# Kernel optimization log

Hardware: AMD Instinct MI355X
Metric: run time of the kernel (lower is better)

The kernel has to match this reference:

```python
import jax, jax.numpy as jnp
import numpy as np

DECAY = 0.99   # LIF membrane decay
INH = 1.625    # lateral inhibition strength (mode='max')


def setup_inputs() -> dict:
    key = jax.random.key(0)
    kx, kw = jax.random.split(key)
    B, Cin, Cout = 8192, 4096, 1024
    x = (jax.random.uniform(kx, (B, Cin)) < 0.2).astype(jnp.float32)
    # weights, then normweight(): clamp to [0,1] and scale each row so row-max == 0.1
    W = jax.random.uniform(kw, (Cout, Cin), dtype=jnp.float32)
    W = W / (W.max(axis=1, keepdims=True) / 0.1)
    return {"x": x, "W": W, "time_window": 10}


def reference(x, W, time_window):
    # current through the bias-free linear layer; constant across timesteps
    i = x @ W.T                                   # (B, Cout)
    # adaptive threshold init: threshold = 3 * max over batch (thre_init branch)
    thr = 3.0 * i.max(axis=0)                     # (Cout,)
    imax = i.max(axis=1, keepdims=True)           # (B, 1), for mode='max' inhibition
    C = i.shape[1]

    def step(mem, _):
        mem = mem * DECAY + i                     # LIF integration
        s = (mem > thr).astype(i.dtype)           # threshold fire
        mem = mem * (1.0 - s)                     # hard reset at all spikers
        row = s.max(axis=1, keepdims=True)        # (B,1) 1 if any neuron in row spiked
        # winner-take-all k=1: keep a single spiking neuron per row (first/argmax)
        wta = jax.nn.one_hot(jnp.argmax(s, axis=1), C, dtype=i.dtype) * row
        # lateral inhibition: subtract inh * max-current from losers in rows that spiked
        mem = mem - INH * imax * (row - wta)
        return mem, wta

    mem0 = jnp.zeros_like(i)
    _, wtas = jax.lax.scan(step, mem0, None, length=time_window)
    return wtas.sum(axis=0)                       # accumulated spikes (B, Cout)
```

## Files before the change

### kernel.cpp

```cpp
#include <hip/hip_runtime.h>
#include <cstdint>

#define B_DIM 8192
#define CIN   4096
#define COUT  1024
#define NPLN  3072

constexpr double W_SCALE   = 83230720.0;
constexpr int    QMAX      = 8323072;
constexpr double INV_SCALE = 0.1 / 8323072.0;

using i32x4 = __attribute__((ext_vector_type(4))) int;

__device__ __forceinline__ void async_copy16(void* lds, const void* g) {
    auto l = (__attribute__((address_space(3))) void*)(uintptr_t)(lds);
    auto p = (const __attribute__((address_space(1))) void*)(uintptr_t)(g);
    __builtin_amdgcn_global_load_lds(p, l, 16, 0, 0);
}

__global__ void prep_x(const float* __restrict__ x, int8_t* __restrict__ Ai) {
    const size_t base = (size_t)blockIdx.x * 1024;
    const float4* xp = (const float4*)x;
    int* op = (int*)Ai;
#pragma unroll
    for (int s = 0; s < 4; ++s) {
        const size_t g = base + s * 256 + threadIdx.x;
        float4 v = xp[g];
        int r = (v.x != 0.f ? 1 : 0) | ((v.y != 0.f ? 1 : 0) << 8) |
                ((v.z != 0.f ? 1 : 0) << 16) | ((v.w != 0.f ? 1 : 0) << 24);
        op[g] = r;
    }
}

__global__ void prep_w(const float* __restrict__ W, int8_t* __restrict__ Bd,
                       unsigned long long* __restrict__ cm) {
    const int idx = blockIdx.x * 256 + threadIdx.x;
    float4 w = ((const float4*)W)[idx];
    float ws[4] = {w.x, w.y, w.z, w.w};
    char dg[3][4];
#pragma unroll
    for (int k = 0; k < 4; ++k) {
        int qv = __double2int_rn((double)ws[k] * W_SCALE);
        qv = max(0, min(QMAX, qv));
        int d0 = ((qv + 128) & 255) - 128; int tq = (qv - d0) >> 8;
        int d1 = ((tq + 128) & 255) - 128; int d2 = (tq - d1) >> 8;
        dg[0][k] = (char)d0; dg[1][k] = (char)d1; dg[2][k] = (char)d2;
    }
    const size_t off = (size_t)idx * 4;
#pragma unroll
    for (int p = 0; p < 3; ++p) {
        char4 c4; c4.x = dg[p][0]; c4.y = dg[p][1]; c4.z = dg[p][2]; c4.w = dg[p][3];
        *(char4*)(Bd + (size_t)p * COUT * CIN + off) = c4;
    }
    if (idx < COUT) cm[idx] = 0ull;
}

__global__ __launch_bounds__(256, 2) void gemm_i8(const int8_t* __restrict__ A,
                                                  const int8_t* __restrict__ Bm,
                                                  int* __restrict__ S) {
    __shared__ alignas(16) int8_t As[128 * 64];
    __shared__ alignas(16) int8_t Bs[128 * 64];
    const int tid  = threadIdx.x;
    const int lane = tid & 63;
    const int wave = tid >> 6;
    const int wr = wave >> 1, wc = wave & 1;
    const int bn = blockIdx.x, bm = blockIdx.y;

    const int r0  = tid >> 2;
    const int c0  = tid & 3;
    const int gc0 = c0 ^ ((r0 >> 1) & 3);
    const int r1  = r0 + 64;
    const int gc1 = c0 ^ ((r1 >> 1) & 3);
    const int8_t* Ag0 = A  + (size_t)(bm * 128 + r0) * CIN + gc0 * 16;
    const int8_t* Ag1 = A  + (size_t)(bm * 128 + r1) * CIN + gc1 * 16;
    const int8_t* Bg0 = Bm + (size_t)(bn * 128 + r0) * CIN + gc0 * 16;
    const int8_t* Bg1 = Bm + (size_t)(bn * 128 + r1) * CIN + gc1 * 16;
    int8_t* AsW = As + wave * 1024;
    int8_t* BsW = Bs + wave * 1024;

    const int mrow = lane & 15;
    const int q    = lane >> 4;
    const int sw   = (mrow >> 1) & 3;
    const int aoff = (wr * 64 + mrow) * 64 + (q ^ sw) * 16;
    const int boff = (wc * 64 + mrow) * 64 + (q ^ sw) * 16;

    i32x4 acc[4][4] = {};
    for (int kc = 0; kc < CIN; kc += 64) {
        __syncthreads();
        async_copy16(AsW,        Ag0 + kc);
        async_copy16(AsW + 4096, Ag1 + kc);
        async_copy16(BsW,        Bg0 + kc);
        async_copy16(BsW + 4096, Bg1 + kc);
        __syncthreads();
        i32x4 a[4], b[4];
#pragma unroll
        for (int t = 0; t < 4; ++t) a[t] = *(const i32x4*)(As + aoff + t * 1024);
#pragma unroll
        for (int t = 0; t < 4; ++t) b[t] = *(const i32x4*)(Bs + boff + t * 1024);
#pragma unroll
        for (int mt = 0; mt < 4; ++mt)
#pragma unroll
            for (int nt = 0; nt < 4; ++nt)
                acc[mt][nt] = __builtin_amdgcn_mfma_i32_16x16x64_i8(a[mt], b[nt], acc[mt][nt], 0, 0, 0);
    }

    const int gm0 = bm * 128 + wr * 64 + q * 4;
    const int gn0 = bn * 128 + wc * 64 + mrow;
#pragma unroll
    for (int mt = 0; mt < 4; ++mt)
#pragma unroll
        for (int nt = 0; nt < 4; ++nt) {
            const int gn = gn0 + nt * 16;
#pragma unroll
            for (int reg = 0; reg < 4; ++reg) {
                const int gm = gm0 + mt * 16 + reg;
                S[(size_t)gm * NPLN + gn] = acc[mt][nt][reg];
            }
        }
}

__global__ void colmax_k(const int* __restrict__ S, unsigned long long* __restrict__ cm) {
    const int j = blockIdx.x * 256 + threadIdx.x;
    const int rbeg = blockIdx.y * 32;
    double m0 = 0.0, m1 = 0.0, m2 = 0.0, m3 = 0.0;
    for (int r = rbeg; r < rbeg + 32; r += 4) {
#pragma unroll
        for (int u = 0; u < 4; ++u) {
            const int* row = S + (size_t)(r + u) * NPLN;
            long long s0 = row[j], s1 = row[COUT + j], s2 = row[2 * COUT + j];
            long long isum = s0 + s1 * 256 + s2 * 65536;
            double v = (double)isum * INV_SCALE;
            if (u == 0) m0 = fmax(m0, v);
            else if (u == 1) m1 = fmax(m1, v);
            else if (u == 2) m2 = fmax(m2, v);
            else m3 = fmax(m3, v);
        }
    }
    double m = fmax(fmax(m0, m1), fmax(m2, m3));
    atomicMax(cm + j, (unsigned long long)__double_as_longlong(m));
}

__global__ void scan_k(const int* __restrict__ S, const unsigned long long* __restrict__ cm,
                       const int* __restrict__ twp, float* __restrict__ out) {
    const int lane = threadIdx.x & 63;
    const int wave = threadIdx.x >> 6;
    const int b = blockIdx.x * 4 + wave;
    const int T = *twp;
    const int4* row = (const int4*)(S + (size_t)b * NPLN);
    const ulonglong2* cm2 = (const ulonglong2*)cm;

    double iv[16], mem[16], thr[16];
    int cnt[16];
    double imax = 0.0;
#pragma unroll
    for (int k = 0; k < 4; ++k) {
        int4 v0 = row[0 * 256 + k * 64 + lane];
        int4 v1 = row[1 * 256 + k * 64 + lane];
        int4 v2 = row[2 * 256 + k * 64 + lane];
        ulonglong2 ca = cm2[k * 128 + 2 * lane];
        ulonglong2 cb = cm2[k * 128 + 2 * lane + 1];
        int a0[4] = {v0.x, v0.y, v0.z, v0.w};
        int a1[4] = {v1.x, v1.y, v1.z, v1.w};
        int a2[4] = {v2.x, v2.y, v2.z, v2.w};
        unsigned long long cs[4] = {ca.x, ca.y, cb.x, cb.y};
#pragma unroll
        for (int w = 0; w < 4; ++w) {
            const int u = k * 4 + w;
            long long isum = (long long)a0[w] + (long long)a1[w] * 256 + (long long)a2[w] * 65536;
            iv[u]  = (double)isum * INV_SCALE;
            thr[u] = 3.0 * __longlong_as_double((long long)cs[w]);
            mem[u] = 0.0; cnt[u] = 0;
            imax = fmax(imax, iv[u]);
        }
    }
#pragma unroll
    for (int d = 32; d >= 1; d >>= 1) imax = fmax(imax, __shfl_xor(imax, d, 64));
    const double h = 1.625 * imax;

    for (int t = 0; t < T; ++t) {
        int first = 0x7fffffff;
        bool sp[16];
#pragma unroll
        for (int u = 0; u < 16; ++u) {
            mem[u] = mem[u] * 0.99 + iv[u];
            sp[u] = mem[u] > thr[u];
            if (sp[u]) {
                const int j = (u >> 2) * 256 + 4 * lane + (u & 3);
                first = min(first, j);
            }
        }
#pragma unroll
        for (int d = 32; d >= 1; d >>= 1) first = min(first, __shfl_xor(first, d, 64));
        const bool rowspike = first < 0x7fffffff;
#pragma unroll
        for (int u = 0; u < 16; ++u) {
            if (sp[u]) mem[u] = 0.0;
            if (rowspike) {
                const int j = (u >> 2) * 256 + 4 * lane + (u & 3);
                if (j == first) cnt[u]++;
                else mem[u] -= h;
            }
        }
    }
    float* ob = out + (size_t)b * COUT;
#pragma unroll
    for (int k = 0; k < 4; ++k) {
        float4 st;
        st.x = (float)cnt[k * 4 + 0];
        st.y = (float)cnt[k * 4 + 1];
        st.z = (float)cnt[k * 4 + 2];
        st.w = (float)cnt[k * 4 + 3];
        ((float4*)(ob + k * 256))[lane] = st;
    }
}

extern "C" void kernel_launch(void* const* d_in, const int* in_sizes, int n_in,
                              void* d_out, int out_size, void* d_ws, size_t ws_size,
                              hipStream_t stream) {
    const float* x  = (const float*)d_in[0];
    const float* W  = (const float*)d_in[1];
    const int*   tw = (const int*)d_in[2];
    float* out = (float*)d_out;

    int8_t* Ai = (int8_t*)d_ws;
    int8_t* Bd = Ai + (size_t)B_DIM * CIN;
    int*    S  = (int*)(Bd + (size_t)NPLN * CIN);
    unsigned long long* cm =
        (unsigned long long*)((int8_t*)S + (size_t)B_DIM * NPLN * 4);

    hipLaunchKernelGGL(prep_x,   dim3(8192),    dim3(256), 0, stream, x, Ai);
    hipLaunchKernelGGL(prep_w,   dim3(4096),    dim3(256), 0, stream, W, Bd, cm);
    hipLaunchKernelGGL(gemm_i8,  dim3(24, 64),  dim3(256), 0, stream, Ai, Bd, S);
    hipLaunchKernelGGL(colmax_k, dim3(4, 256),  dim3(256), 0, stream, S, cm);
    hipLaunchKernelGGL(scan_k,   dim3(2048),    dim3(256), 0, stream, S, cm, tw, out);
}
```

Baseline: 389.4 us.

## Fuse digit-plane recombination and column max into GEMM epilogue

The GEMM tile is reorganized so each block computes all three weight digit planes for the same 64 output columns. The epilogue can then recombine the planes into a double current and compute per-column maxima with shuffles and atomicMax. This removes the separate colmax kernel and its full re-read of the int32 plane buffer, and the scan kernel reads one double per element instead of three ints. In exchange the GEMM holds more accumulators, its tile shape changes, and the stored intermediate is 8 bytes per element instead of 12.

```diff
diff --git a/kernel.cpp b/kernel.cpp
--- a/kernel.cpp
+++ b/kernel.cpp
@@ -4,7 +4,6 @@
 #define B_DIM 8192
 #define CIN   4096
 #define COUT  1024
-#define NPLN  3072
 
 constexpr double W_SCALE   = 83230720.0;
 constexpr int    QMAX      = 8323072;
@@ -55,11 +54,12 @@
     if (idx < COUT) cm[idx] = 0ull;
 }
 
-__global__ __launch_bounds__(256, 2) void gemm_i8(const int8_t* __restrict__ A,
-                                                  const int8_t* __restrict__ Bm,
-                                                  int* __restrict__ S) {
+__global__ __launch_bounds__(256, 2) void gemm_i8f(const int8_t* __restrict__ A,
+                                                   const int8_t* __restrict__ Bm,
+                                                   double* __restrict__ Sd,
+                                                   unsigned long long* __restrict__ cm) {
     __shared__ alignas(16) int8_t As[128 * 64];
-    __shared__ alignas(16) int8_t Bs[128 * 64];
+    __shared__ alignas(16) int8_t Bs[3 * 64 * 64];
     const int tid  = threadIdx.x;
     const int lane = tid & 63;
     const int wave = tid >> 6;
@@ -68,85 +68,82 @@
 
     const int r0  = tid >> 2;
     const int c0  = tid & 3;
-    const int gc0 = c0 ^ ((r0 >> 1) & 3);
+    const int gc  = c0 ^ ((r0 >> 1) & 3);
     const int r1  = r0 + 64;
     const int gc1 = c0 ^ ((r1 >> 1) & 3);
-    const int8_t* Ag0 = A  + (size_t)(bm * 128 + r0) * CIN + gc0 * 16;
-    const int8_t* Ag1 = A  + (size_t)(bm * 128 + r1) * CIN + gc1 * 16;
-    const int8_t* Bg0 = Bm + (size_t)(bn * 128 + r0) * CIN + gc0 * 16;
-    const int8_t* Bg1 = Bm + (size_t)(bn * 128 + r1) * CIN + gc1 * 16;
+    const int8_t* Ag0 = A + (size_t)(bm * 128 + r0) * CIN + gc * 16;
+    const int8_t* Ag1 = A + (size_t)(bm * 128 + r1) * CIN + gc1 * 16;
+    const int8_t* Bg0 = Bm + (size_t)(0 * COUT + bn * 64 + r0) * CIN + gc * 16;
+    const int8_t* Bg1 = Bm + (size_t)(1 * COUT + bn * 64 + r0) * CIN + gc * 16;
+    const int8_t* Bg2 = Bm + (size_t)(2 * COUT + bn * 64 + r0) * CIN + gc * 16;
     int8_t* AsW = As + wave * 1024;
     int8_t* BsW = Bs + wave * 1024;
 
     const int mrow = lane & 15;
     const int q    = lane >> 4;
     const int sw   = (mrow >> 1) & 3;
-    const int aoff = (wr * 64 + mrow) * 64 + (q ^ sw) * 16;
-    const int boff = (wc * 64 + mrow) * 64 + (q ^ sw) * 16;
-
-    i32x4 acc[4][4] = {};
+    const int koff = (q ^ sw) * 16;
+    const int aoff = (wr * 64 + mrow) * 64 + koff;
+    const int boff = (wc * 32 + mrow) * 64 + koff;
+
+    i32x4 acc[3][4][2] = {};
     for (int kc = 0; kc < CIN; kc += 64) {
         __syncthreads();
         async_copy16(AsW,        Ag0 + kc);
         async_copy16(AsW + 4096, Ag1 + kc);
         async_copy16(BsW,        Bg0 + kc);
         async_copy16(BsW + 4096, Bg1 + kc);
+        async_copy16(BsW + 8192, Bg2 + kc);
         __syncthreads();
-        i32x4 a[4], b[4];
+        i32x4 a[4], b[3][2];
 #pragma unroll
         for (int t = 0; t < 4; ++t) a[t] = *(const i32x4*)(As + aoff + t * 1024);
 #pragma unroll
-        for (int t = 0; t < 4; ++t) b[t] = *(const i32x4*)(Bs + boff + t * 1024);
+        for (int p = 0; p < 3; ++p)
+#pragma unroll
+            for (int nt = 0; nt < 2; ++nt)
+                b[p][nt] = *(const i32x4*)(Bs + p * 4096 + boff + nt * 1024);
 #pragma unroll
         for (int mt = 0; mt < 4; ++mt)
 #pragma unroll
-            for (int nt = 0; nt < 4; ++nt)
-                acc[mt][nt] = __builtin_amdgcn_mfma_i32_16x16x64_i8(a[mt], b[nt], acc[mt][nt], 0, 0, 0);
+            for (int p = 0; p < 3; ++p)
+#pragma unroll
+                for (int nt = 0; nt < 2; ++nt)
+                    acc[p][mt][nt] =
+                        __builtin_amdgcn_mfma_i32_16x16x64_i8(a[mt], b[p][nt], acc[p][mt][nt], 0, 0, 0);
     }
 
     const int gm0 = bm * 128 + wr * 64 + q * 4;
-    const int gn0 = bn * 128 + wc * 64 + mrow;
-#pragma unroll
-    for (int mt = 0; mt < 4; ++mt)
-#pragma unroll
-        for (int nt = 0; nt < 4; ++nt) {
-            const int gn = gn0 + nt * 16;
+    const int gn0 = bn * 64 + wc * 32 + mrow;
+#pragma unroll
+    for (int nt = 0; nt < 2; ++nt) {
+        const int gn = gn0 + nt * 16;
+        double cmax = 0.0;
+#pragma unroll
+        for (int mt = 0; mt < 4; ++mt)
 #pragma unroll
             for (int reg = 0; reg < 4; ++reg) {
-                const int gm = gm0 + mt * 16 + reg;
-                S[(size_t)gm * NPLN + gn] = acc[mt][nt][reg];
+                long long isum = (long long)acc[0][mt][nt][reg]
+                               + 256LL   * (long long)acc[1][mt][nt][reg]
+                               + 65536LL * (long long)acc[2][mt][nt][reg];
+                double v = (double)isum * INV_SCALE;
+                Sd[(size_t)(gm0 + mt * 16 + reg) * COUT + gn] = v;
+                cmax = fmax(cmax, v);
             }
-        }
-}
-
-__global__ void colmax_k(const int* __restrict__ S, unsigned long long* __restrict__ cm) {
-    const int j = blockIdx.x * 256 + threadIdx.x;
-    const int rbeg = blockIdx.y * 32;
-    double m0 = 0.0, m1 = 0.0, m2 = 0.0, m3 = 0.0;
-    for (int r = rbeg; r < rbeg + 32; r += 4) {
-#pragma unroll
-        for (int u = 0; u < 4; ++u) {
-            const int* row = S + (size_t)(r + u) * NPLN;
-            long long s0 = row[j], s1 = row[COUT + j], s2 = row[2 * COUT + j];
-            long long isum = s0 + s1 * 256 + s2 * 65536;
-            double v = (double)isum * INV_SCALE;
-            if (u == 0) m0 = fmax(m0, v);
-            else if (u == 1) m1 = fmax(m1, v);
-            else if (u == 2) m2 = fmax(m2, v);
-            else m3 = fmax(m3, v);
-        }
-    }
-    double m = fmax(fmax(m0, m1), fmax(m2, m3));
-    atomicMax(cm + j, (unsigned long long)__double_as_longlong(m));
-}
-
-__global__ void scan_k(const int* __restrict__ S, const unsigned long long* __restrict__ cm,
+        cmax = fmax(cmax, __shfl_xor(cmax, 16, 64));
+        cmax = fmax(cmax, __shfl_xor(cmax, 32, 64));
+        if (lane < 16)
+            atomicMax(cm + gn, (unsigned long long)__double_as_longlong(cmax));
+    }
+}
+
+__global__ void scan_k(const double* __restrict__ Sd, const unsigned long long* __restrict__ cm,
                        const int* __restrict__ twp, float* __restrict__ out) {
     const int lane = threadIdx.x & 63;
     const int wave = threadIdx.x >> 6;
     const int b = blockIdx.x * 4 + wave;
     const int T = *twp;
-    const int4* row = (const int4*)(S + (size_t)b * NPLN);
+    const double2* row2 = (const double2*)(Sd + (size_t)b * COUT);
     const ulonglong2* cm2 = (const ulonglong2*)cm;
 
     double iv[16], mem[16], thr[16];
@@ -154,20 +151,16 @@
     double imax = 0.0;
 #pragma unroll
     for (int k = 0; k < 4; ++k) {
-        int4 v0 = row[0 * 256 + k * 64 + lane];
-        int4 v1 = row[1 * 256 + k * 64 + lane];
-        int4 v2 = row[2 * 256 + k * 64 + lane];
+        double2 d0 = row2[k * 128 + 2 * lane];
+        double2 d1 = row2[k * 128 + 2 * lane + 1];
         ulonglong2 ca = cm2[k * 128 + 2 * lane];
         ulonglong2 cb = cm2[k * 128 + 2 * lane + 1];
-        int a0[4] = {v0.x, v0.y, v0.z, v0.w};
-        int a1[4] = {v1.x, v1.y, v1.z, v1.w};
-        int a2[4] = {v2.x, v2.y, v2.z, v2.w};
+        double vs[4] = {d0.x, d0.y, d1.x, d1.y};
         unsigned long long cs[4] = {ca.x, ca.y, cb.x, cb.y};
 #pragma unroll
         for (int w = 0; w < 4; ++w) {
             const int u = k * 4 + w;
-            long long isum = (long long)a0[w] + (long long)a1[w] * 256 + (long long)a2[w] * 65536;
-            iv[u]  = (double)isum * INV_SCALE;
+            iv[u]  = vs[w];
             thr[u] = 3.0 * __longlong_as_double((long long)cs[w]);
             mem[u] = 0.0; cnt[u] = 0;
             imax = fmax(imax, iv[u]);
@@ -224,13 +217,12 @@
 
     int8_t* Ai = (int8_t*)d_ws;
     int8_t* Bd = Ai + (size_t)B_DIM * CIN;
-    int*    S  = (int*)(Bd + (size_t)NPLN * CIN);
+    double* Sd = (double*)(Bd + (size_t)3 * COUT * CIN);
     unsigned long long* cm =
-        (unsigned long long*)((int8_t*)S + (size_t)B_DIM * NPLN * 4);
-
-    hipLaunchKernelGGL(prep_x,   dim3(8192),    dim3(256), 0, stream, x, Ai);
-    hipLaunchKernelGGL(prep_w,   dim3(4096),    dim3(256), 0, stream, W, Bd, cm);
-    hipLaunchKernelGGL(gemm_i8,  dim3(24, 64),  dim3(256), 0, stream, Ai, Bd, S);
-    hipLaunchKernelGGL(colmax_k, dim3(4, 256),  dim3(256), 0, stream, S, cm);
-    hipLaunchKernelGGL(scan_k,   dim3(2048),    dim3(256), 0, stream, S, cm, tw, out);
-}
+        (unsigned long long*)((int8_t*)Sd + (size_t)B_DIM * COUT * 8);
+
+    hipLaunchKernelGGL(prep_x,   dim3(8192),   dim3(256), 0, stream, x, Ai);
+    hipLaunchKernelGGL(prep_w,   dim3(4096),   dim3(256), 0, stream, W, Bd, cm);
+    hipLaunchKernelGGL(gemm_i8f, dim3(16, 64), dim3(256), 0, stream, Ai, Bd, Sd, cm);
+    hipLaunchKernelGGL(scan_k,   dim3(2048),   dim3(256), 0, stream, Sd, cm, tw, out);
+}
```

After: 390.0 us. Within noise of the previous version (+0.2%).
